# Kernel optimization log

Hardware: AMD Instinct MI355X
Metric: run time of the kernel (lower is better)

Reference implementation:

```python
import jax, jax.numpy as jnp
import numpy as np

WS = 7  # window_size


def _conv1x1(x, W, b):
    # 1x1 conv == channel-mixing matmul. W: [out_c, in_c], b: [out_c]
    return jnp.einsum('oc,bchw->bohw', W, x) + b[None, :, None, None]


def _window_flatten(t, ws):
    # [b, ch, H, W] -> [b, ch*nh*nw, ws*ws], matching torch unfold+contiguous+view
    b, ch, H, W = t.shape
    nh, nw = H // ws, W // ws
    t = t.reshape(b, ch, nh, ws, nw, ws).transpose(0, 1, 2, 4, 3, 5)  # [b,ch,nh,nw,ws,ws]
    return t.reshape(b, ch * nh * nw, ws * ws)


def setup_inputs() -> dict:
    key = jax.random.key(0)
    ks = jax.random.split(key, 7)
    b, c, h, w = 8, 256, 160, 160
    c8 = c // 8
    x = jax.random.normal(ks[0], (b, c, h, w), dtype=jnp.float32)
    Wq = jax.random.normal(ks[1], (c8, c), dtype=jnp.float32) * (1.0 / np.sqrt(c))
    bq = jnp.zeros((c8,), dtype=jnp.float32)
    Wk = jax.random.normal(ks[2], (c8, c), dtype=jnp.float32) * (1.0 / np.sqrt(c))
    bk = jnp.zeros((c8,), dtype=jnp.float32)
    Wv = jax.random.normal(ks[3], (c, c), dtype=jnp.float32) * (1.0 / np.sqrt(c))
    bv = jnp.zeros((c,), dtype=jnp.float32)
    return {"x": x, "Wq": Wq, "bq": bq, "Wk": Wk, "bk": bk, "Wv": Wv, "bv": bv}


def reference(x, Wq, bq, Wk, bk, Wv, bv):
    b, c, h, w = x.shape
    ws = WS
    pad_h = (ws - h % ws) % ws
    pad_w = (ws - w % ws) % ws
    xp = jnp.pad(x, ((0, 0), (0, 0), (0, pad_h), (0, pad_w)), mode='reflect')
    H, W = xp.shape[2], xp.shape[3]

    q = _window_flatten(_conv1x1(xp, Wq, bq), ws)  # [b, c8*nwin, 49]
    k = _window_flatten(_conv1x1(xp, Wk, bk), ws)  # [b, c8*nwin, 49]
    v = _window_flatten(_conv1x1(xp, Wv, bv), ws)  # [b, c*nwin, 49]

    # attn = softmax(q^T @ k) over last dim; reduction axis is channels*windows
    attn = jax.nn.softmax(jnp.einsum('bnp,bnq->bpq', q, k), axis=-1)  # [b,49,49]
    # out = v @ attn^T  -> out[b,m,i] = sum_j v[b,m,j] * attn[b,i,j]
    out = jnp.einsum('bmj,bij->bmi', v, attn)  # [b, c*nwin, 49]

    # faithful to torch .view(b, c, H, W) on contiguous [b,c,nh,nw,ws,ws] memory
    out = out.reshape(b, c, H, W)
    return out[:, :, :h, :w]
```

## Files before the change

kernel.cpp:

```cpp
#include <hip/hip_runtime.h>

#define C_ 256
#define HIN 160
#define NH 23
#define NWIN 529
#define OPLANE 25600

#define G3 3
#define NG3 177
#define NPX 160
#define XSP 40
#define QST2 164

typedef short bf16x8 __attribute__((ext_vector_type(8)));
typedef float f32x4 __attribute__((ext_vector_type(4)));
typedef unsigned short u16x4 __attribute__((ext_vector_type(4)));

__device__ __forceinline__ unsigned short f2bf(float f) {
    union { float f; unsigned u; } v; v.f = f;
    unsigned r = v.u + 0x7FFFu + ((v.u >> 16) & 1u);
    return (unsigned short)(r >> 16);
}

__global__ void kprep(const float* __restrict__ Wq, const float* __restrict__ Wk,
                      const float* __restrict__ Wv, unsigned short* __restrict__ WvB,
                      unsigned short* __restrict__ W2h, unsigned short* __restrict__ W2l,
                      float* __restrict__ S) {
    int t = blockIdx.x * 256 + threadIdx.x;
    if (t < 65536) WvB[t] = f2bf(Wv[t]);
    if (t < 16384) {
        int och = t >> 8, c = t & 255;
        float w = (och < 32) ? Wq[och * 256 + c] : Wk[(och - 32) * 256 + c];
        unsigned short h = f2bf(w);
        union { unsigned u; float f; } uh; uh.u = (unsigned)h << 16;
        W2h[t] = h;
        W2l[t] = f2bf(w - uh.f);
    }
    if (t < 8 * 2401) S[t] = 0.f;
}

__launch_bounds__(256, 2)
__global__ void k12(const float* __restrict__ x, const unsigned short* __restrict__ W2h,
                    const unsigned short* __restrict__ W2l, const float* __restrict__ bq,
                    const float* __restrict__ bk, float* __restrict__ S) {
    __shared__ __align__(16) unsigned short Xh[NPX * XSP];
    __shared__ __align__(16) unsigned short Xl[NPX * XSP];
    __shared__ float QKs[64 * QST2];

    int t = threadIdx.x;
    int g = blockIdx.x;
    int b = g & 7, grp = g >> 3;
    int win0 = grp * G3;
    const float* xb = x + (long)b * C_ * OPLANE;

    int c8 = t >> 5;
    int j32 = t & 31;
    const float* bases[5];
    bool bval[5];
#pragma unroll
    for (int m = 0; m < 5; ++m) {
        int px = j32 + 32 * m;
        int w = px / 49, p = px - w * 49;
        int win = win0 + w;
        bool v = (px < 147) && (win < NWIN);
        bval[m] = v;
        int wy = win / NH, wx = win - wy * NH;
        int gy = wy * 7 + p / 7, gx = wx * 7 + p % 7;
        int sy = (gy < HIN) ? gy : 158;
        int sx = (gx < HIN) ? gx : 158;
        bases[m] = v ? (xb + sy * HIN + sx) : xb;
    }

    int lane = t & 63, r16 = lane & 15, quad = lane >> 4, q8 = quad * 8;
    int w = t >> 6;

    f32x4 zero = {0.f, 0.f, 0.f, 0.f};
    f32x4 acc[10];
#pragma unroll
    for (int nt = 0; nt < 10; ++nt) acc[nt] = zero;

    float pf[20];
#pragma unroll
    for (int k = 0; k < 4; ++k)
#pragma unroll
        for (int m = 0; m < 5; ++m)
            pf[k * 5 + m] = bval[m] ? bases[m][(long)(c8 + 8 * k) * OPLANE] : 0.f;

    for (int c0 = 0; c0 < 256; c0 += 32) {
#pragma unroll
        for (int k = 0; k < 4; ++k) {
            int cl = c8 + 8 * k;
#pragma unroll
            for (int m = 0; m < 5; ++m) {
                int px = j32 + 32 * m;
                float v = pf[k * 5 + m];
                unsigned short h = f2bf(v);
                union { unsigned u; float f; } uh; uh.u = (unsigned)h << 16;
                Xh[px * XSP + cl] = h;
                Xl[px * XSP + cl] = f2bf(v - uh.f);
            }
        }
        __syncthreads();
        if (c0 + 32 < 256) {
            int c1 = c0 + 32;
#pragma unroll
            for (int k = 0; k < 4; ++k)
#pragma unroll
                for (int m = 0; m < 5; ++m)
                    pf[k * 5 + m] = bval[m] ? bases[m][(long)(c1 + c8 + 8 * k) * OPLANE] : 0.f;
        }
        bf16x8 ah = *(const bf16x8*)&W2h[(16 * w + r16) * 256 + c0 + q8];
        bf16x8 al = *(const bf16x8*)&W2l[(16 * w + r16) * 256 + c0 + q8];
        __builtin_amdgcn_s_setprio(1);
#pragma unroll
        for (int nt = 0; nt < 10; ++nt) {
            bf16x8 bh = *(const bf16x8*)&Xh[(nt * 16 + r16) * XSP + q8];
            bf16x8 bl = *(const bf16x8*)&Xl[(nt * 16 + r16) * XSP + q8];
            acc[nt] = __builtin_amdgcn_mfma_f32_16x16x32_bf16(ah, bh, acc[nt], 0, 0, 0);
            acc[nt] = __builtin_amdgcn_mfma_f32_16x16x32_bf16(ah, bl, acc[nt], 0, 0, 0);
            acc[nt] = __builtin_amdgcn_mfma_f32_16x16x32_bf16(al, bh, acc[nt], 0, 0, 0);
        }
        __builtin_amdgcn_s_setprio(0);
        __syncthreads();
    }

    float bias[4];
#pragma unroll
    for (int r = 0; r < 4; ++r) {
        int och = 16 * w + quad * 4 + r;
        bias[r] = (och < 32) ? bq[och] : bk[och - 32];
    }
#pragma unroll
    for (int nt = 0; nt < 10; ++nt) {
        int px = nt * 16 + r16;
        int wof = px / 49;
        bool v = (px < 147) && (win0 + wof < NWIN);
#pragma unroll
        for (int r = 0; r < 4; ++r) {
            int och = 16 * w + quad * 4 + r;
            QKs[och * QST2 + px] = v ? (acc[nt][r] + bias[r]) : 0.f;
        }
    }
    __syncthreads();

    if (t < 169) {
        int p0 = (t / 13) * 4, q0 = (t % 13) * 4;
        float s[4][4];
#pragma unroll
        for (int r = 0; r < 4; ++r)
#pragma unroll
            for (int cc = 0; cc < 4; ++cc) s[r][cc] = 0.f;
        for (int wi = 0; wi < G3; ++wi) {
            for (int ch = 0; ch < 32; ++ch) {
                const float* qr = &QKs[ch * QST2 + wi * 49 + p0];
                const float* kr = &QKs[(32 + ch) * QST2 + wi * 49 + q0];
                float qv[4] = {qr[0], qr[1], qr[2], qr[3]};
                float kv[4] = {kr[0], kr[1], kr[2], kr[3]};
#pragma unroll
                for (int r = 0; r < 4; ++r)
#pragma unroll
                    for (int cc = 0; cc < 4; ++cc)
                        s[r][cc] = fmaf(qv[r], kv[cc], s[r][cc]);
            }
        }
        float* sp = S + b * 2401;
#pragma unroll
        for (int r = 0; r < 4; ++r) {
            int pp = p0 + r;
            if (pp < 49) {
#pragma unroll
                for (int cc = 0; cc < 4; ++cc) {
                    int qq = q0 + cc;
                    if (qq < 49) atomicAdd(&sp[pp * 49 + qq], s[r][cc]);
                }
            }
        }
    }
}

__global__ void ksoft(const float* __restrict__ S, unsigned short* __restrict__ attnP) {
    int b = blockIdx.x, t = threadIdx.x;
    unsigned short* row = attnP + (b * 64 + t) * 64;
    if (t < 49) {
        const float* sr = S + b * 2401 + t * 49;
        float m = -1e30f;
        for (int j = 0; j < 49; ++j) m = fmaxf(m, sr[j]);
        float den = 0.f;
        for (int j = 0; j < 49; ++j) den += expf(sr[j] - m);
        float inv = 1.f / den;
        for (int j = 0; j < 49; ++j) row[j] = f2bf(expf(sr[j] - m) * inv);
        for (int j = 49; j < 64; ++j) row[j] = 0;
    } else {
        for (int j = 0; j < 64; ++j) row[j] = 0;
    }
}

#define XCS 72
#define YTS 264
#define OTS2 50
__launch_bounds__(256, 4)
__global__ void k3(const float* __restrict__ x, const unsigned short* __restrict__ WvB,
                   const unsigned short* __restrict__ attnP, const float* __restrict__ bv,
                   float* __restrict__ out) {
    __shared__ __align__(16) unsigned short U[256 * XCS];
    unsigned short* Xc = U;
    unsigned short* Yt = U;

    int t = threadIdx.x;
    int bw = blockIdx.x;
    int b = bw & 7;
    int win = bw >> 3;
    int wy = win / NH, wx = win % NH;
    int lane = t & 63;
    int r16 = lane & 15, quad = lane >> 4, q8 = quad * 8;
    int w64 = (t >> 6) * 64;

    const float* xb = x + (long)b * C_ * OPLANE;

    {
        int j = t & 63;
        bool jvalid = (j < 49);
        int gy = wy * 7 + j / 7, gx = wx * 7 + j % 7;
        int sy = (gy < HIN) ? gy : 158;
        int sx = (gx < HIN) ? gx : 158;
        const float* xs = xb + sy * HIN + sx;
        int cb = t >> 6;
#pragma unroll
        for (int gg = 0; gg < 4; ++gg) {
            float v[16];
#pragma unroll
            for (int i = 0; i < 16; ++i)
                v[i] = jvalid ? xs[(long)(cb + 4 * (gg * 16 + i)) * OPLANE] : 0.f;
#pragma unroll
            for (int i = 0; i < 16; ++i)
                Xc[(cb + 4 * (gg * 16 + i)) * XCS + j] = f2bf(v[i]);
        }
    }
    __syncthreads();

    f32x4 zero = {0.f, 0.f, 0.f, 0.f};
    f32x4 acc[4][4];
#pragma unroll
    for (int i = 0; i < 4; ++i)
#pragma unroll
        for (int j = 0; j < 4; ++j) acc[i][j] = zero;

    __builtin_amdgcn_s_setprio(1);
#pragma unroll
    for (int half = 0; half < 2; ++half) {
        int k0 = half * 32;
        bf16x8 a[4], bfr[4];
#pragma unroll
        for (int mt = 0; mt < 4; ++mt)
            a[mt] = *(const bf16x8*)&Xc[(w64 + mt * 16 + r16) * XCS + k0 + q8];
#pragma unroll
        for (int nt = 0; nt < 4; ++nt)
            bfr[nt] = *(const bf16x8*)&attnP[(b * 64 + nt * 16 + r16) * 64 + k0 + q8];
#pragma unroll
        for (int mt = 0; mt < 4; ++mt)
#pragma unroll
            for (int nt = 0; nt < 4; ++nt)
                acc[mt][nt] = __builtin_amdgcn_mfma_f32_16x16x32_bf16(a[mt], bfr[nt], acc[mt][nt], 0, 0, 0);
    }
    __builtin_amdgcn_s_setprio(0);
    __syncthreads();

#pragma unroll
    for (int mt = 0; mt < 4; ++mt) {
        int cb = w64 + mt * 16 + quad * 4;
#pragma unroll
        for (int nt = 0; nt < 4; ++nt) {
            int ic = nt * 16 + r16;
            u16x4 pk;
            pk[0] = f2bf(acc[mt][nt][0]);
            pk[1] = f2bf(acc[mt][nt][1]);
            pk[2] = f2bf(acc[mt][nt][2]);
            pk[3] = f2bf(acc[mt][nt][3]);
            *(u16x4*)&Yt[ic * YTS + cb] = pk;
        }
    }
    __syncthreads();

#pragma unroll
    for (int i = 0; i < 4; ++i)
#pragma unroll
        for (int j = 0; j < 4; ++j) acc[i][j] = zero;

    __builtin_amdgcn_s_setprio(1);
#pragma unroll
    for (int ks = 0; ks < 8; ++ks) {
        int k0 = ks * 32;
        bf16x8 a[4], bb2[4];
#pragma unroll
        for (int mt = 0; mt < 4; ++mt)
            a[mt] = *(const bf16x8*)&WvB[(w64 + mt * 16 + r16) * 256 + k0 + q8];
#pragma unroll
        for (int nt = 0; nt < 4; ++nt)
            bb2[nt] = *(const bf16x8*)&Yt[(nt * 16 + r16) * YTS + k0 + q8];
#pragma unroll
        for (int mt = 0; mt < 4; ++mt)
#pragma unroll
            for (int nt = 0; nt < 4; ++nt)
                acc[mt][nt] = __builtin_amdgcn_mfma_f32_16x16x32_bf16(a[mt], bb2[nt], acc[mt][nt], 0, 0, 0);
    }
    __builtin_amdgcn_s_setprio(0);
    __syncthreads();

    float* Os = (float*)U + (t >> 6) * (32 * OTS2);
    float* ob = out + (long)b * C_ * OPLANE;
    int f0 = win * 49;
    int y0 = f0 / 161, x0 = f0 - y0 * 161;
#pragma unroll
    for (int sub = 0; sub < 2; ++sub) {
#pragma unroll
        for (int mt2 = 0; mt2 < 2; ++mt2) {
            int mt = sub * 2 + mt2;
            int clb = mt2 * 16 + quad * 4;
            int chb = w64 + mt * 16 + quad * 4;
            float bvl[4];
#pragma unroll
            for (int r = 0; r < 4; ++r) bvl[r] = bv[chb + r];
#pragma unroll
            for (int nt = 0; nt < 4; ++nt) {
                int i = nt * 16 + r16;
                if (i < 49) {
#pragma unroll
                    for (int r = 0; r < 4; ++r)
                        Os[(clb + r) * OTS2 + i] = acc[mt][nt][r] + bvl[r];
                }
            }
        }
        for (int idx = lane; idx < 32 * 49; idx += 64) {
            int cl = idx / 49, jj = idx - cl * 49;
            int xx = x0 + jj, yy = y0;
            if (xx >= 161) { ++yy; xx -= 161; }
            if (xx < 160 && yy < 160) {
                int ch = w64 + sub * 32 + cl;
                ob[ch * OPLANE + yy * 160 + xx] = Os[cl * OTS2 + jj];
            }
        }
    }
}

extern "C" void kernel_launch(void* const* d_in, const int* in_sizes, int n_in,
                              void* d_out, int out_size, void* d_ws, size_t ws_size,
                              hipStream_t stream) {
    const float* x  = (const float*)d_in[0];
    const float* Wq = (const float*)d_in[1];
    const float* bq = (const float*)d_in[2];
    const float* Wk = (const float*)d_in[3];
    const float* bk = (const float*)d_in[4];
    const float* Wv = (const float*)d_in[5];
    const float* bv = (const float*)d_in[6];
    float* out = (float*)d_out;

    char* ws = (char*)d_ws;
    unsigned short* WvB   = (unsigned short*)(ws);
    unsigned short* W2h   = (unsigned short*)(ws + 131072);
    unsigned short* W2l   = (unsigned short*)(ws + 163840);
    float* S              = (float*)(ws + 196608);
    unsigned short* attnP = (unsigned short*)(ws + 273440);

    kprep<<<dim3(256), dim3(256), 0, stream>>>(Wq, Wk, Wv, WvB, W2h, W2l, S);
    k12<<<dim3(8 * NG3), dim3(256), 0, stream>>>(x, W2h, W2l, bq, bk, S);
    ksoft<<<dim3(8), dim3(64), 0, stream>>>(S, attnP);
    k3<<<dim3(8 * NWIN), dim3(256), 0, stream>>>(x, WvB, attnP, bv, out);
}
```

Before: 606.1 us.

## Load x directly into MFMA A-fragments, skipping LDS staging in k3

The k3 kernel no longer stages the x window tile through shared memory as bf16. Each lane now gathers its 8 fp32 values per fragment straight from global memory using a small per-block pixel offset table. It then packs them with v_cvt_pk_bf16_f32 into MFMA operands. This removes an LDS write/read round trip and one barrier and shrinks shared memory, but the global gathers are strided and less coalesced. The softmax kernel is also unrolled and now keeps the row in registers, so exp is computed once per element.

Result: slower. 675.1 us (+11.4%).

```diff
diff --git a/kernel.cpp b/kernel.cpp
--- a/kernel.cpp
+++ b/kernel.cpp
@@ -20,6 +20,12 @@
     union { float f; unsigned u; } v; v.f = f;
     unsigned r = v.u + 0x7FFFu + ((v.u >> 16) & 1u);
     return (unsigned short)(r >> 16);
+}
+
+__device__ __forceinline__ unsigned cvtpk(float lo, float hi) {
+    unsigned r;
+    asm("v_cvt_pk_bf16_f32 %0, %1, %2" : "=v"(r) : "v"(lo), "v"(hi));
+    return r;
 }
 
 __global__ void kprep(const float* __restrict__ Wq, const float* __restrict__ Wk,
@@ -183,28 +189,33 @@
     unsigned short* row = attnP + (b * 64 + t) * 64;
     if (t < 49) {
         const float* sr = S + b * 2401 + t * 49;
-        float m = -1e30f;
-        for (int j = 0; j < 49; ++j) m = fmaxf(m, sr[j]);
+        float v[49];
+#pragma unroll
+        for (int j = 0; j < 49; ++j) v[j] = sr[j];
+        float m = v[0];
+#pragma unroll
+        for (int j = 1; j < 49; ++j) m = fmaxf(m, v[j]);
         float den = 0.f;
-        for (int j = 0; j < 49; ++j) den += expf(sr[j] - m);
+#pragma unroll
+        for (int j = 0; j < 49; ++j) { v[j] = expf(v[j] - m); den += v[j]; }
         float inv = 1.f / den;
-        for (int j = 0; j < 49; ++j) row[j] = f2bf(expf(sr[j] - m) * inv);
+#pragma unroll
+        for (int j = 0; j < 49; ++j) row[j] = f2bf(v[j] * inv);
+#pragma unroll
         for (int j = 49; j < 64; ++j) row[j] = 0;
     } else {
         for (int j = 0; j < 64; ++j) row[j] = 0;
     }
 }
 
-#define XCS 72
 #define YTS 264
 #define OTS2 50
 __launch_bounds__(256, 4)
 __global__ void k3(const float* __restrict__ x, const unsigned short* __restrict__ WvB,
                    const unsigned short* __restrict__ attnP, const float* __restrict__ bv,
                    float* __restrict__ out) {
-    __shared__ __align__(16) unsigned short U[256 * XCS];
-    unsigned short* Xc = U;
-    unsigned short* Yt = U;
+    __shared__ __align__(16) unsigned short U[64 * YTS];
+    __shared__ int OffT[64];
 
     int t = threadIdx.x;
     int bw = blockIdx.x;
@@ -217,26 +228,25 @@
 
     const float* xb = x + (long)b * C_ * OPLANE;
 
-    {
-        int j = t & 63;
-        bool jvalid = (j < 49);
-        int gy = wy * 7 + j / 7, gx = wx * 7 + j % 7;
+    if (t < 64) {
+        int j = t;
+        int py = j / 7, px = j % 7;
+        int gy = wy * 7 + py, gx = wx * 7 + px;
         int sy = (gy < HIN) ? gy : 158;
         int sx = (gx < HIN) ? gx : 158;
-        const float* xs = xb + sy * HIN + sx;
-        int cb = t >> 6;
-#pragma unroll
-        for (int gg = 0; gg < 4; ++gg) {
-            float v[16];
-#pragma unroll
-            for (int i = 0; i < 16; ++i)
-                v[i] = jvalid ? xs[(long)(cb + 4 * (gg * 16 + i)) * OPLANE] : 0.f;
-#pragma unroll
-            for (int i = 0; i < 16; ++i)
-                Xc[(cb + 4 * (gg * 16 + i)) * XCS + j] = f2bf(v[i]);
-        }
+        OffT[t] = (j < 49) ? (sy * HIN + sx) : 0;
     }
     __syncthreads();
+
+    int offs[16];
+#pragma unroll
+    for (int k = 0; k < 8; ++k) {
+        offs[k]     = OffT[q8 + k];
+        offs[8 + k] = OffT[32 + q8 + k];
+    }
+    int cof[4];
+#pragma unroll
+    for (int mt = 0; mt < 4; ++mt) cof[mt] = (w64 + mt * 16 + r16) * OPLANE;
 
     f32x4 zero = {0.f, 0.f, 0.f, 0.f};
     f32x4 acc[4][4];
@@ -245,26 +255,37 @@
 #pragma unroll
         for (int j = 0; j < 4; ++j) acc[i][j] = zero;
 
-    __builtin_amdgcn_s_setprio(1);
 #pragma unroll
     for (int half = 0; half < 2; ++half) {
-        int k0 = half * 32;
         bf16x8 a[4], bfr[4];
 #pragma unroll
-        for (int mt = 0; mt < 4; ++mt)
-            a[mt] = *(const bf16x8*)&Xc[(w64 + mt * 16 + r16) * XCS + k0 + q8];
+        for (int mt = 0; mt < 4; ++mt) {
+            float v[8];
+#pragma unroll
+            for (int k = 0; k < 8; ++k) v[k] = xb[cof[mt] + offs[half * 8 + k]];
+            if (half == 1) {
+#pragma unroll
+                for (int k = 0; k < 8; ++k)
+                    if (q8 + k >= 17) v[k] = 0.f;
+            }
+            union { bf16x8 h; unsigned u[4]; } pk;
+#pragma unroll
+            for (int k = 0; k < 4; ++k) pk.u[k] = cvtpk(v[2 * k], v[2 * k + 1]);
+            a[mt] = pk.h;
+        }
 #pragma unroll
         for (int nt = 0; nt < 4; ++nt)
-            bfr[nt] = *(const bf16x8*)&attnP[(b * 64 + nt * 16 + r16) * 64 + k0 + q8];
+            bfr[nt] = *(const bf16x8*)&attnP[(b * 64 + nt * 16 + r16) * 64 + half * 32 + q8];
+        __builtin_amdgcn_s_setprio(1);
 #pragma unroll
         for (int mt = 0; mt < 4; ++mt)
 #pragma unroll
             for (int nt = 0; nt < 4; ++nt)
                 acc[mt][nt] = __builtin_amdgcn_mfma_f32_16x16x32_bf16(a[mt], bfr[nt], acc[mt][nt], 0, 0, 0);
-    }
-    __builtin_amdgcn_s_setprio(0);
-    __syncthreads();
-
+        __builtin_amdgcn_s_setprio(0);
+    }
+
+    unsigned short* Yt = U;
 #pragma unroll
     for (int mt = 0; mt < 4; ++mt) {
         int cb = w64 + mt * 16 + quad * 4;
```
